# Optimization experiments

Measured on AMD Instinct MI355X. Metric: run time of the kernel, lower is better.

## Reference

```python
import jax, jax.numpy as jnp
import numpy as np
from jax import lax

# ---- static config (mirrors cfg) ----
ACT_SIZE = 768
GROUP_SIZES = [2048, 2048, 4096, 8192, 16384]
DICT_SIZE = sum(GROUP_SIZES)            # 32768
GROUP_IDX = np.concatenate([[0], np.cumsum(GROUP_SIZES)]).tolist()
TOP_K = 32
TOP_K_AUX = 512
L1_COEFF = 0.0003
AUX_PENALTY = 0.03125
N_DEAD = 5.0
THRESH_LR = 0.01
BATCH = 2048


def setup_inputs() -> dict:
    key = jax.random.key(0)
    k1, k2, k3, k4 = jax.random.split(key, 4)
    x = jax.random.normal(k1, (BATCH, ACT_SIZE), dtype=jnp.float32)
    W_enc = jax.random.normal(k2, (ACT_SIZE, DICT_SIZE), dtype=jnp.float32) * 0.02
    W_dec = jax.random.normal(k3, (DICT_SIZE, ACT_SIZE), dtype=jnp.float32)
    W_dec = W_dec / jnp.linalg.norm(W_dec, axis=-1, keepdims=True)  # unit-norm rows as in __init__
    num_batches_not_active = jax.random.randint(k4, (DICT_SIZE,), 0, 10).astype(jnp.float32)
    threshold = jnp.float32(0.0)
    return {"x": x, "W_enc": W_enc, "W_dec": W_dec, "b_dec": jnp.zeros((ACT_SIZE,), jnp.float32),
            "num_batches_not_active": num_batches_not_active, "threshold": threshold}


def reference(x, W_enc, W_dec, b_dec, num_batches_not_active, threshold):
    B, D = x.shape[0], DICT_SIZE
    # ---- preprocess (input_unit_norm=True) ----
    x_mean = x.mean(axis=-1, keepdims=True)
    x_std = jnp.std(x, axis=-1, keepdims=True, ddof=1)  # torch .std is unbiased
    xn = (x - x_mean) / (x_std + 1e-5)

    x_cent = xn - b_dec
    # ---- encode + global batch top-k (training path) ----
    acts = jax.nn.relu(x_cent @ W_enc)                  # [B, D]
    flat = acts.reshape(-1)
    k = TOP_K * B
    vals, idx = lax.top_k(flat, k)
    acts_topk = jnp.zeros_like(flat).at[idx].set(vals).reshape(B, D)

    # threshold EMA update (no_grad in torch)
    atk = lax.stop_gradient(acts_topk)
    pos = atk > 0
    min_pos = jnp.min(jnp.where(pos, atk, jnp.inf))
    new_threshold = jnp.where(pos.any(), (1 - THRESH_LR) * threshold + THRESH_LR * min_pos, threshold)

    # ---- matryoshka group decode ----
    x_reconstruct = jnp.broadcast_to(b_dec, xn.shape)
    inters = []
    for i in range(len(GROUP_SIZES)):
        s, e = GROUP_IDX[i], GROUP_IDX[i + 1]
        x_reconstruct = acts_topk[:, s:e] @ W_dec[s:e, :] + x_reconstruct
        inters.append(x_reconstruct)

    # ---- inactive-feature bookkeeping (no_grad) ----
    col_sums = lax.stop_gradient(acts_topk).sum(axis=0)
    nb = jnp.where(col_sums > 0, 0.0, num_batches_not_active + 1.0)

    # ---- loss dict ----
    total_l2 = jnp.mean((b_dec - xn) ** 2)
    l2s = jnp.stack([jnp.mean((r - xn) ** 2) for r in inters])
    total_l2 = total_l2 + l2s.sum()
    mean_l2 = total_l2 / (len(inters) + 1)
    x_var = jnp.var(xn, ddof=1)
    fvu = mean_l2 / (x_var + 1e-10)
    l1_norm = jnp.abs(acts_topk).sum(-1).mean()
    l0_norm = (acts_topk > 0).astype(jnp.float32).sum(-1).mean()
    l1_loss = L1_COEFF * l1_norm

    # ---- auxiliary loss over dead features ----
    dead = nb >= N_DEAD                                  # [D] bool, static count >> TOP_K_AUX here
    residual = xn - x_reconstruct
    masked = jnp.where(dead[None, :], acts, -jnp.inf)    # restrict top-k to dead features
    vals_a, idx_a = lax.top_k(masked, TOP_K_AUX)         # per-row top-k, [B, TOP_K_AUX]
    vals_a = jnp.where(jnp.isfinite(vals_a), vals_a, 0.0)
    acts_aux = jnp.zeros((B, D), acts.dtype).at[jnp.arange(B)[:, None], idx_a].set(vals_a)
    aux_reconstruct = acts_aux @ W_dec
    aux_mse = jnp.mean((aux_reconstruct - residual) ** 2)
    aux_loss = jnp.where(jnp.abs(aux_reconstruct).sum() > 0, AUX_PENALTY * aux_mse, 0.0)

    loss = mean_l2 + l1_loss + aux_loss
    num_dead_features = (nb > N_DEAD).sum()
    sae_out = x_reconstruct * x_std + x_mean

    return (sae_out, acts_topk, loss, l1_loss, mean_l2, l2s.min(), l2s.max(),
            l0_norm, l1_norm, aux_loss, new_threshold, fvu, num_dead_features)
```

## Files before the change

kernel.cpp:

```cpp
#include <hip/hip_runtime.h>
#include <stdint.h>

#define DEVFN static __device__ __forceinline__

typedef unsigned short u16;
typedef unsigned long long u64;
typedef short short8 __attribute__((ext_vector_type(8)));
typedef float vf4 __attribute__((ext_vector_type(4)));

constexpr int B = 2048;
constexpr int DIN = 768;
constexpr int D = 32768;
constexpr int NDI = B * D;
constexpr unsigned TOPK_TOTAL = 65536u;
constexpr int TOPK_AUX = 512;
constexpr int ROWCAP = 512;
constexpr int CANDCAP = 2097152;
constexpr int CSTAGE = 4096;
constexpr int TIECAP = 4096;
constexpr int SCAP = 3072;
constexpr int NREP = 16;

constexpr size_t OFF_HIST1  = 0;
constexpr size_t OFF_HIST2  = 131072;
constexpr size_t OFF_HIST3  = 262144;
constexpr size_t OFF_HIST4  = 393216;
constexpr size_t OFF_SCALU  = 458752;
constexpr size_t OFF_SCALD  = 459008;
constexpr size_t OFF_ROWCNT = 459264;
constexpr size_t OFF_AUXCNT = 467456;
constexpr size_t OFF_COLACT = 475648;
constexpr size_t ZERO_BYTES = 606720;
constexpr size_t OFF_XN    = ZERO_BYTES;
constexpr size_t OFF_RES   = OFF_XN   + 6291456;
constexpr size_t OFF_RMEAN = OFF_RES  + 6291456;
constexpr size_t OFF_RSTD  = OFF_RMEAN + 8192;
constexpr size_t OFF_XNCB  = OFF_RSTD + 8192;
constexpr size_t OFF_DEAD  = OFF_XNCB + 3145728;
constexpr size_t OFF_DMASK = OFF_DEAD + 131072;
constexpr size_t OFF_DBASE = OFF_DMASK + 4096;
constexpr size_t OFF_RLC   = OFF_DBASE + 2048;
constexpr size_t OFF_RLV   = OFF_RLC  + 4194304;
constexpr size_t OFF_AXC   = OFF_RLV  + 4194304;
constexpr size_t OFF_AXV   = OFF_AXC  + 4194304;
constexpr size_t OFF_CANDI = OFF_AXV  + 4194304;
constexpr size_t OFF_CANDV = OFF_CANDI + (size_t)CANDCAP * 4;
constexpr size_t OFF_TIEB  = OFF_CANDV + (size_t)CANDCAP * 4;
constexpr size_t OFF_WT    = OFF_TIEB + (size_t)TIECAP * 4;


DEVFN u16 f2bf(float f) {
  unsigned u = __float_as_uint(f);
  unsigned r = (u + 0x7FFFu + ((u >> 16) & 1u)) >> 16;
  return (u16)r;
}
DEVFN float b2f(u16 h) { return __uint_as_float(((unsigned)h) << 16); }

DEVFN float bsumf(float v, float* red) {
  int t = threadIdx.x;
  red[t] = v; __syncthreads();
  for (int o = 128; o > 0; o >>= 1) { if (t < o) red[t] += red[t + o]; __syncthreads(); }
  float r = red[0]; __syncthreads();
  return r;
}
DEVFN unsigned bsumu(unsigned v, unsigned* red) {
  int t = threadIdx.x;
  red[t] = v; __syncthreads();
  for (int o = 128; o > 0; o >>= 1) { if (t < o) red[t] += red[t + o]; __syncthreads(); }
  unsigned r = red[0]; __syncthreads();
  return r;
}

DEVFN void findBin(const unsigned* hist, int nb, unsigned K, unsigned base,
                   unsigned* sscan, int* s_b, unsigned* s_cnt)
{
  int t = threadIdx.x;
  int chunk = nb >> 8;
  int hi = nb - 1 - t * chunk;
  unsigned p = 0;
  for (int k = 0; k < chunk; ++k) p += hist[hi - k];
  sscan[t] = p; __syncthreads();
  for (int o = 1; o < 256; o <<= 1) {
    unsigned xx = (t >= o) ? sscan[t - o] : 0u; __syncthreads();
    sscan[t] += xx; __syncthreads();
  }
  unsigned incl = sscan[t], excl = incl - p;
  unsigned cum = base + excl;
  if (base + incl >= K && cum < K) {
    unsigned acc = cum;
    for (int k = 0; k < chunk; ++k) {
      unsigned h = hist[hi - k];
      if (acc + h >= K) { *s_b = hi - k; *s_cnt = acc; break; }
      acc += h;
    }
  }
  __syncthreads();
}

__global__ __launch_bounds__(256) void k_rowstats(
    const float* __restrict__ x, const float* __restrict__ bdec,
    float* __restrict__ xn, u16* __restrict__ xncb,
    float* __restrict__ rmean, float* __restrict__ rstd, double* scalD)
{
  __shared__ float red[256];
  const int row = blockIdx.x, t = threadIdx.x;
  const float* xr = x + (size_t)row * DIN;
  float v0 = xr[t], v1 = xr[t + 256], v2 = xr[t + 512];
  float mean = bsumf(v0 + v1 + v2, red) * (1.0f / DIN);
  float d0 = v0 - mean, d1 = v1 - mean, d2 = v2 - mean;
  float var = bsumf(d0 * d0 + d1 * d1 + d2 * d2, red) * (1.0f / (DIN - 1));
  float sd = sqrtf(var);
  float inv = 1.0f / (sd + 1e-5f);
  float n0 = d0 * inv, n1 = d1 * inv, n2 = d2 * inv;
  size_t o = (size_t)row * DIN;
  xn[o + t] = n0; xn[o + t + 256] = n1; xn[o + t + 512] = n2;
  float b0 = bdec[t], b1 = bdec[t + 256], b2 = bdec[t + 512];
  xncb[o + t] = f2bf(n0 - b0); xncb[o + t + 256] = f2bf(n1 - b1); xncb[o + t + 512] = f2bf(n2 - b2);
  if (t == 0) { rmean[row] = mean; rstd[row] = sd; }
  float sxn = bsumf(n0 + n1 + n2, red);
  float ssq = bsumf(n0 * n0 + n1 * n1 + n2 * n2, red);
  float e0 = b0 - n0, e1 = b1 - n1, e2 = b2 - n2;
  float sq0 = bsumf(e0 * e0 + e1 * e1 + e2 * e2, red);
  if (t == 0) {
    atomicAdd(&scalD[1], (double)sxn);
    atomicAdd(&scalD[2], (double)ssq);
    atomicAdd(&scalD[3], (double)sq0);
  }
}

__global__ __launch_bounds__(256) void k_wt(const float* __restrict__ W, u16* __restrict__ Wt)
{
  __shared__ float tl[64][65];
  const int t = threadIdx.x;
  const int n0 = blockIdx.x * 64, k0 = blockIdx.y * 64;
  const int rr = t >> 6, cc = t & 63;
#pragma unroll
  for (int r = 0; r < 16; ++r) {
    int kk = r * 4 + rr;
    tl[kk][cc] = W[(size_t)(k0 + kk) * D + n0 + cc];
  }
  __syncthreads();
#pragma unroll
  for (int r = 0; r < 16; ++r) {
    int nn = r * 4 + rr;
    Wt[(size_t)(n0 + nn) * DIN + k0 + cc] = f2bf(tl[cc][nn]);
  }
}

__global__ __launch_bounds__(256) void k_wdecb(const float4* __restrict__ W4, u16* __restrict__ Wb)
{
  int stride = gridDim.x * blockDim.x;
  const int n4 = (D * DIN) / 4;
  for (int i = blockIdx.x * 256 + threadIdx.x; i < n4; i += stride) {
    float4 f = W4[i];
    unsigned p0 = (unsigned)f2bf(f.x) | ((unsigned)f2bf(f.y) << 16);
    unsigned p1 = (unsigned)f2bf(f.z) | ((unsigned)f2bf(f.w) << 16);
    uint2 q; q.x = p0; q.y = p1;
    *(uint2*)&Wb[(size_t)i * 4] = q;
  }
}

__global__ __launch_bounds__(256) void k_gemm(const u16* __restrict__ A,
                                              const u16* __restrict__ Bt,
                                              float* __restrict__ C,
                                              unsigned* __restrict__ hist16)
{
  __shared__ __align__(16) char lds[32768];
  const int tid = threadIdx.x, lane = tid & 63, wid = tid >> 6;
  const int bn = blockIdx.x * 128, bm = blockIdx.y * 128;

  const char* pA[4]; const char* pB[4];
#pragma unroll
  for (int i = 0; i < 4; ++i) {
    int G = i * 256 + wid * 64 + lane;
    int r = G >> 3, c = (G & 7) ^ (r & 7);
    pA[i] = (const char*)(A + (size_t)(bm + r) * DIN + c * 8);
    pB[i] = (const char*)(Bt + (size_t)(bn + r) * DIN + c * 8);
  }
  int aoff[2][4], boff[2][4];
#pragma unroll
  for (int kc = 0; kc < 2; ++kc)
#pragma unroll
    for (int i = 0; i < 4; ++i) {
      int cs = kc * 4 + (lane >> 4);
      int rA = (wid >> 1) * 64 + i * 16 + (lane & 15);
      aoff[kc][i] = rA * 128 + ((cs ^ (rA & 7)) * 16);
      int rB = (wid & 1) * 64 + i * 16 + (lane & 15);
      boff[kc][i] = 16384 + rB * 128 + ((cs ^ (rB & 7)) * 16);
    }

  vf4 acc[4][4];
#pragma unroll
  for (int i = 0; i < 4; ++i)
#pragma unroll
    for (int j = 0; j < 4; ++j) acc[i][j] = (vf4)0.f;

  for (int ks = 0; ks < 12; ++ks) {
    __syncthreads();
#pragma unroll
    for (int i = 0; i < 4; ++i) {
      __builtin_amdgcn_global_load_lds(
          (const __attribute__((address_space(1))) void*)pA[i],
          (__attribute__((address_space(3))) void*)(lds + (i * 256 + wid * 64) * 16), 16, 0, 0);
      __builtin_amdgcn_global_load_lds(
          (const __attribute__((address_space(1))) void*)pB[i],
          (__attribute__((address_space(3))) void*)(lds + 16384 + (i * 256 + wid * 64) * 16), 16, 0, 0);
      pA[i] += 128; pB[i] += 128;
    }
    __syncthreads();
#pragma unroll
    for (int kc = 0; kc < 2; ++kc) {
      short8 av[4], bv[4];
#pragma unroll
      for (int i = 0; i < 4; ++i) {
        av[i] = *(const short8*)(lds + aoff[kc][i]);
        bv[i] = *(const short8*)(lds + boff[kc][i]);
      }
#pragma unroll
      for (int i = 0; i < 4; ++i)
#pragma unroll
        for (int j = 0; j < 4; ++j)
          acc[i][j] = __builtin_amdgcn_mfma_f32_16x16x32_bf16(av[i], bv[j], acc[i][j], 0, 0, 0);
    }
  }

  unsigned* h = (unsigned*)lds;
  __syncthreads();
  for (int j = tid; j < 2048; j += 256) h[j] = 0;
  __syncthreads();

  const int r0 = bm + (wid >> 1) * 64 + (lane >> 4) * 4;
  const int c0 = bn + (wid & 1) * 64 + (lane & 15);
#pragma unroll
  for (int i = 0; i < 4; ++i)
#pragma unroll
    for (int j = 0; j < 4; ++j) {
      float* cp = C + (size_t)(r0 + i * 16) * D + c0 + j * 16;
#pragma unroll
      for (int q = 0; q < 4; ++q) {
        float v = fmaxf(acc[i][j][q], 0.f);
        cp[(size_t)q * D] = v;
        if (v >= 1.0f) atomicAdd(&h[__float_as_uint(v) >> 21], 1u);
      }
    }
  __syncthreads();
  unsigned* dst = hist16 + (size_t)(blockIdx.x & (NREP - 1)) * 2048;
  for (int j = 508 + tid; j < 2048; j += 256) {
    unsigned c = h[j];
    if (c) atomicAdd(&dst[j], c);
  }
}

__global__ __launch_bounds__(256) void k_scan1a(unsigned* scalU, const unsigned* __restrict__ h16)
{
  __shared__ unsigned hsum[2048];
  __shared__ unsigned sscan[256];
  __shared__ int s_b; __shared__ unsigned s_cnt;
  int t = threadIdx.x;
  for (int j = t; j < 2048; j += 256) {
    unsigned s = 0;
#pragma unroll
    for (int r = 0; r < NREP; ++r) s += h16[r * 2048 + j];
    hsum[j] = s;
  }
  if (t == 0) { s_b = 0; s_cnt = 0; }
  __syncthreads();
  unsigned p = 0;
  for (int j = 508 + t; j < 2048; j += 256) p += hsum[j];
  unsigned total = bsumu(p, sscan);
  if (total >= TOPK_TOTAL) {
    findBin(hsum, 2048, TOPK_TOTAL, 0u, sscan, &s_b, &s_cnt);
    if (t == 0) { scalU[0] = (unsigned)s_b; scalU[1] = s_cnt; scalU[13] = 0u; }
  } else if (t == 0) scalU[13] = 1u;
}

__global__ __launch_bounds__(256) void k_histfull(const float4* __restrict__ a4,
    const unsigned* __restrict__ scalU, unsigned* __restrict__ h16)
{
  if (scalU[13] == 0u) return;
  __shared__ unsigned lh[4][2048];
  for (int j = threadIdx.x; j < 8192; j += 256) ((unsigned*)lh)[j] = 0;
  __syncthreads();
  unsigned* mylh = lh[threadIdx.x & 3];
  int stride = gridDim.x * blockDim.x;
  for (int i = blockIdx.x * 256 + threadIdx.x; i < NDI / 4; i += stride) {
    float4 f = a4[i];
    if (f.x > 0.f) atomicAdd(&mylh[__float_as_uint(f.x) >> 21], 1u);
    if (f.y > 0.f) atomicAdd(&mylh[__float_as_uint(f.y) >> 21], 1u);
    if (f.z > 0.f) atomicAdd(&mylh[__float_as_uint(f.z) >> 21], 1u);
    if (f.w > 0.f) atomicAdd(&mylh[__float_as_uint(f.w) >> 21], 1u);
  }
  __syncthreads();
  unsigned* dst = h16 + (size_t)(blockIdx.x & (NREP - 1)) * 2048;
  for (int j = threadIdx.x; j < 2048; j += 256) {
    unsigned c = lh[0][j] + lh[1][j] + lh[2][j] + lh[3][j];
    if (c) atomicAdd(&dst[j], c);
  }
}

__global__ __launch_bounds__(256) void k_scan1b(unsigned* scalU, const unsigned* __restrict__ h16)
{
  if (scalU[13] == 0u) return;
  __shared__ unsigned hsum[2048];
  __shared__ unsigned sscan[256];
  __shared__ int s_b; __shared__ unsigned s_cnt;
  int t = threadIdx.x;
  for (int j = t; j < 2048; j += 256) {
    unsigned s = 0;
#pragma unroll
    for (int r = 0; r < NREP; ++r) s += h16[r * 2048 + j];
    hsum[j] = s;
  }
  if (t == 0) { s_b = 0; s_cnt = 0; }
  __syncthreads();
  findBin(hsum, 2048, TOPK_TOTAL, 0u, sscan, &s_b, &s_cnt);
  if (t == 0) { scalU[0] = (unsigned)s_b; scalU[1] = s_cnt; }
}

__global__ __launch_bounds__(256) void k_compact(const float4* __restrict__ a4,
    unsigned* scalU, unsigned* __restrict__ candI, float* __restrict__ candV)
{
  __shared__ unsigned sIdx[CSTAGE];
  __shared__ float sVal[CSTAGE];
  __shared__ unsigned sCnt, sBase;
  if (threadIdx.x == 0) sCnt = 0;
  __syncthreads();
  unsigned b1 = scalU[0];
  int stride = gridDim.x * blockDim.x;
  for (int i = blockIdx.x * 256 + threadIdx.x; i < NDI / 4; i += stride) {
    float4 f = a4[i];
    float vv[4] = {f.x, f.y, f.z, f.w};
#pragma unroll
    for (int c = 0; c < 4; ++c) {
      float v = vv[c];
      if (v > 0.f && (__float_as_uint(v) >> 21) >= b1) {
        unsigned p = atomicAdd(&sCnt, 1u);
        if (p < (unsigned)CSTAGE) { sIdx[p] = (unsigned)(i * 4 + c); sVal[p] = v; }
        else {
          unsigned g = atomicAdd(&scalU[12], 1u);
          if (g < (unsigned)CANDCAP) { candI[g] = (unsigned)(i * 4 + c); candV[g] = v; }
        }
      }
    }
  }
  __syncthreads();
  unsigned n = sCnt < (unsigned)CSTAGE ? sCnt : (unsigned)CSTAGE;
  if (threadIdx.x == 0) sBase = atomicAdd(&scalU[12], n);
  __syncthreads();
  unsigned base = sBase;
  for (unsigned j = threadIdx.x; j < n; j += 256) {
    unsigned g = base + j;
    if (g < (unsigned)CANDCAP) { candI[g] = sIdx[j]; candV[g] = sVal[j]; }
  }
}

__global__ __launch_bounds__(256) void k_rhist2(const unsigned* __restrict__ scalU,
    const float* __restrict__ candV, unsigned* __restrict__ h16)
{
  __shared__ unsigned lh[2048];
  for (int j = threadIdx.x; j < 2048; j += 256) lh[j] = 0;
  __syncthreads();
  unsigned b1 = scalU[0];
  int n = (int)scalU[12]; if (n > CANDCAP) n = CANDCAP;
  int stride = gridDim.x * blockDim.x;
  for (int j = blockIdx.x * 256 + threadIdx.x; j < n; j += stride) {
    unsigned u = __float_as_uint(candV[j]);
    if ((u >> 21) == b1) atomicAdd(&lh[(u >> 10) & 0x7FFu], 1u);
  }
  __syncthreads();
  unsigned* dst = h16 + (size_t)(blockIdx.x & (NREP - 1)) * 2048;
  for (int j = threadIdx.x; j < 2048; j += 256) {
    unsigned c = lh[j];
    if (c) atomicAdd(&dst[j], c);
  }
}

__global__ __launch_bounds__(256) void k_rscan2(unsigned* scalU, const unsigned* __restrict__ h16)
{
  __shared__ unsigned hsum[2048];
  __shared__ unsigned sscan[256];
  __shared__ int s_b; __shared__ unsigned s_cnt;
  int t = threadIdx.x;
  for (int j = t; j < 2048; j += 256) {
    unsigned s = 0;
#pragma unroll
    for (int r = 0; r < NREP; ++r) s += h16[r * 2048 + j];
    hsum[j] = s;
  }
  if (t == 0) { s_b = 0; s_cnt = 0; }
  __syncthreads();
  findBin(hsum, 2048, TOPK_TOTAL, scalU[1], sscan, &s_b, &s_cnt);
  if (t == 0) { scalU[2] = (unsigned)s_b; scalU[3] = s_cnt; }
}

__global__ __launch_bounds__(256) void k_rhist3(const unsigned* __restrict__ scalU,
    const float* __restrict__ candV, unsigned* __restrict__ h16)
{
  __shared__ unsigned lh[1024];
  for (int j = threadIdx.x; j < 1024; j += 256) lh[j] = 0;
  __syncthreads();
  unsigned b1 = scalU[0], b2 = scalU[2];
  int n = (int)scalU[12]; if (n > CANDCAP) n = CANDCAP;
  int stride = gridDim.x * blockDim.x;
  for (int j = blockIdx.x * 256 + threadIdx.x; j < n; j += stride) {
    unsigned u = __float_as_uint(candV[j]);
    if ((u >> 21) == b1 && ((u >> 10) & 0x7FFu) == b2) atomicAdd(&lh[u & 0x3FFu], 1u);
  }
  __syncthreads();
  unsigned* dst = h16 + (size_t)(blockIdx.x & (NREP - 1)) * 1024;
  for (int j = threadIdx.x; j < 1024; j += 256) {
    unsigned c = lh[j];
    if (c) atomicAdd(&dst[j], c);
  }
}

__global__ __launch_bounds__(256) void k_rscan3(unsigned* scalU, const unsigned* __restrict__ h16)
{
  __shared__ unsigned hsum[1024];
  __shared__ unsigned sscan[256];
  __shared__ int s_b; __shared__ unsigned s_cnt;
  int t = threadIdx.x;
  for (int j = t; j < 1024; j += 256) {
    unsigned s = 0;
#pragma unroll
    for (int r = 0; r < NREP; ++r) s += h16[r * 1024 + j];
    hsum[j] = s;
  }
  if (t == 0) { s_b = 0; s_cnt = 0; }
  __syncthreads();
  findBin(hsum, 1024, TOPK_TOTAL, scalU[3], sscan, &s_b, &s_cnt);
  if (t == 0) {
    unsigned cut = (scalU[0] << 21) | (scalU[2] << 10) | (unsigned)s_b;
    scalU[4] = cut; scalU[5] = s_cnt; scalU[6] = TOPK_TOTAL - s_cnt;
  }
}

__global__ __launch_bounds__(256) void k_tiecol(unsigned* scalU,
    const unsigned* __restrict__ candI, const float* __restrict__ candV,
    unsigned* __restrict__ tieB)
{
  unsigned cut = scalU[4];
  int n = (int)scalU[12]; if (n > CANDCAP) n = CANDCAP;
  int stride = gridDim.x * blockDim.x;
  for (int j = blockIdx.x * 256 + threadIdx.x; j < n; j += stride) {
    if (__float_as_uint(candV[j]) == cut) {
      unsigned p = atomicAdd(&scalU[14], 1u);
      if (p < (unsigned)TIECAP) tieB[p] = candI[j];
    }
  }
}

__global__ __launch_bounds__(256) void k_tieres(unsigned* scalU, const unsigned* __restrict__ tieB)
{
  __shared__ unsigned tbuf[TIECAP];
  __shared__ int sthr;
  int t = threadIdx.x;
  int m = (int)scalU[14]; if (m > TIECAP) m = TIECAP;
  int need = (int)scalU[6];
  for (int j = t; j < m; j += 256) tbuf[j] = tieB[j];
  if (t == 0) sthr = 0x7FFFFFFF;
  __syncthreads();
  if (need < m) {
    for (int ci = t; ci < m; ci += 256) {
      unsigned me = tbuf[ci];
      int r = 0;
      for (int j = 0; j < m; ++j) r += (tbuf[j] < me) ? 1 : 0;
      if (r == need - 1) sthr = (int)me;
    }
  }
  __syncthreads();
  if (t == 0) scalU[7] = (unsigned)sthr;
}

__global__ __launch_bounds__(256) void k_s1b(unsigned* scalU,
    const unsigned* __restrict__ candI, const float* __restrict__ candV,
    unsigned* rowCnt, unsigned* rlc, float* rlv, unsigned* colAct, double* scalD)
{
  __shared__ float redf[256];
  __shared__ unsigned redu[256];
  unsigned cut = scalU[4]; int tthr = (int)scalU[7];
  int n = (int)scalU[12]; if (n > CANDCAP) n = CANDCAP;
  float l1 = 0.f; unsigned l0 = 0;
  int stride = gridDim.x * blockDim.x;
  for (int j = blockIdx.x * 256 + threadIdx.x; j < n; j += stride) {
    float v = candV[j];
    unsigned u = __float_as_uint(v);
    unsigned idx = candI[j];
    if (u > cut || (u == cut && (int)idx <= tthr)) {
      int row = (int)(idx >> 15), col = (int)(idx & (D - 1));
      unsigned slot = atomicAdd(&rowCnt[row], 1u);
      if (slot < ROWCAP) {
        rlc[(size_t)row * ROWCAP + slot] = (unsigned)col;
        rlv[(size_t)row * ROWCAP + slot] = v;
      }
      colAct[col] = 1u;
      l1 += v; l0++;
    }
  }
  float l1s = bsumf(l1, redf);
  unsigned l0s = bsumu(l0, redu);
  if (threadIdx.x == 0) { atomicAdd(&scalD[0], (double)l1s); atomicAdd(&scalU[9], l0s); }
}

__global__ __launch_bounds__(256) void k_scatter(const unsigned* __restrict__ scalU,
    const unsigned* __restrict__ candI, const float* __restrict__ candV, float* __restrict__ acts)
{
  unsigned cut = scalU[4]; int tthr = (int)scalU[7];
  int n = (int)scalU[12]; if (n > CANDCAP) n = CANDCAP;
  int stride = gridDim.x * blockDim.x;
  for (int j = blockIdx.x * 256 + threadIdx.x; j < n; j += stride) {
    float v = candV[j];
    unsigned u = __float_as_uint(v);
    unsigned idx = candI[j];
    if (u > cut || (u == cut && (int)idx <= tthr)) acts[idx] = v;
  }
}

__global__ __launch_bounds__(256) void k_dead(const unsigned* __restrict__ colAct,
    const float* __restrict__ nbna, unsigned* deadCols, unsigned* scalU,
    u64* __restrict__ dmask, unsigned* __restrict__ dbase)
{
  __shared__ unsigned scan[256];
  __shared__ unsigned svd;
  const int t = threadIdx.x;
  if (t == 0) svd = 0;
  __syncthreads();
  const int c0 = t * 128;
  u64 w0 = 0, w1 = 0;
  unsigned vd = 0;
  for (int i = 0; i < 64; ++i) {
    int c = c0 + i;
    bool act = colAct[c] != 0;
    float f = nbna[c] + 1.0f;
    if (!act && f >= 5.0f) w0 |= (1ull << i);
    vd += (!act && f > 5.0f) ? 1u : 0u;
  }
  for (int i = 0; i < 64; ++i) {
    int c = c0 + 64 + i;
    bool act = colAct[c] != 0;
    float f = nbna[c] + 1.0f;
    if (!act && f >= 5.0f) w1 |= (1ull << i);
    vd += (!act && f > 5.0f) ? 1u : 0u;
  }
  unsigned cnt = (unsigned)(__popcll(w0) + __popcll(w1));
  scan[t] = cnt; __syncthreads();
  for (int o = 1; o < 256; o <<= 1) {
    unsigned xx = (t >= o) ? scan[t - o] : 0u; __syncthreads();
    scan[t] += xx; __syncthreads();
  }
  unsigned p = scan[t] - cnt;
  dmask[2 * t] = w0; dmask[2 * t + 1] = w1;
  dbase[2 * t] = p; dbase[2 * t + 1] = p + (unsigned)__popcll(w0);
  atomicAdd(&svd, vd);
  __syncthreads();
  if (t == 255) scalU[10] = scan[255];
  if (t == 0) scalU[11] = svd;
  (void)deadCols;
}

__global__ __launch_bounds__(256) void k_auxsel(const float* __restrict__ acts,
    const unsigned* __restrict__ scalU, const u64* __restrict__ dmask,
    unsigned* auxC, float* auxV, unsigned* auxN)
{
  __shared__ u64 smask[512];
  __shared__ unsigned hist[2048];
  __shared__ unsigned sscan[256];
  __shared__ float tval[SCAP];
  __shared__ unsigned tcol[SCAP];
  __shared__ int s_b; __shared__ unsigned s_cnt;
  __shared__ unsigned s_sel, s_tm;
  const int row = blockIdx.x, t = threadIdx.x;
  const float4* arow4 = (const float4*)(acts + (size_t)row * D);

  for (int j = t; j < 512; j += 256) smask[j] = dmask[j];
  for (int j = t; j < 2048; j += 256) hist[j] = 0;
  if (t == 0) { s_sel = 0; s_tm = 0; s_b = 0; s_cnt = 0; }
  __syncthreads();

  unsigned pcnt = 0;
  for (int j = t; j < D / 4; j += 256) {
    float4 f = arow4[j];
    u64 w = smask[j >> 4];
    int sh = (j & 15) * 4;
    float vv[4] = {f.x, f.y, f.z, f.w};
#pragma unroll
    for (int c = 0; c < 4; ++c) {
      if (((w >> (sh + c)) & 1ull) && vv[c] > 0.f) {
        pcnt++;
        atomicAdd(&hist[__float_as_uint(vv[c]) >> 21], 1u);
      }
    }
  }
  unsigned P = bsumu(pcnt, sscan);
  unsigned* outC = auxC + (size_t)row * TOPK_AUX;
  float* outV = auxV + (size_t)row * TOPK_AUX;

  if (P <= (unsigned)TOPK_AUX) {
    for (int j = t; j < D / 4; j += 256) {
      float4 f = arow4[j];
      u64 w = smask[j >> 4];
      int sh = (j & 15) * 4;
      float vv[4] = {f.x, f.y, f.z, f.w};
#pragma unroll
      for (int c = 0; c < 4; ++c)
        if (((w >> (sh + c)) & 1ull) && vv[c] > 0.f) {
          unsigned s = atomicAdd(&s_sel, 1u);
          outC[s] = (unsigned)(j * 4 + c); outV[s] = vv[c];
        }
    }
    __syncthreads();
    if (t == 0) auxN[row] = s_sel;
    return;
  }

  __syncthreads();
  findBin(hist, 2048, (unsigned)TOPK_AUX, 0u, sscan, &s_b, &s_cnt);
  unsigned b1 = (unsigned)s_b, c1 = s_cnt;

  for (int j = t; j < D / 4; j += 256) {
    float4 f = arow4[j];
    u64 w = smask[j >> 4];
    int sh = (j & 15) * 4;
    float vv[4] = {f.x, f.y, f.z, f.w};
#pragma unroll
    for (int c = 0; c < 4; ++c) {
      if (((w >> (sh + c)) & 1ull) && vv[c] > 0.f) {
        unsigned bin = __float_as_uint(vv[c]) >> 21;
        if (bin > b1) {
          unsigned s = atomicAdd(&s_sel, 1u);
          outC[s] = (unsigned)(j * 4 + c); outV[s] = vv[c];
        } else if (bin == b1) {
          unsigned p = atomicAdd(&s_tm, 1u);
          if (p < (unsigned)SCAP) { tcol[p] = (unsigned)(j * 4 + c); tval[p] = vv[c]; }
        }
      }
    }
  }
  __syncthreads();
  int m = (int)s_tm;

  if (m <= SCAP) {
    for (int j = t; j < 2048; j += 256) hist[j] = 0;
    if (t == 0) { s_b = 0; s_cnt = 0; }
    __syncthreads();
    for (int j = t; j < m; j += 256)
      atomicAdd(&hist[(__float_as_uint(tval[j]) >> 10) & 0x7FFu], 1u);
    __syncthreads();
    findBin(hist, 2048, (unsigned)TOPK_AUX, c1, sscan, &s_b, &s_cnt);
    unsigned b2 = (unsigned)s_b, c2 = s_cnt;
    for (int j = t; j < 1024; j += 256) hist[j] = 0;
    if (t == 0) { s_b = 0; s_cnt = 0; }
    __syncthreads();
    for (int j = t; j < m; j += 256) {
      unsigned u = __float_as_uint(tval[j]);
      if (((u >> 10) & 0x7FFu) == b2) atomicAdd(&hist[u & 0x3FFu], 1u);
    }
    __syncthreads();
    findBin(hist, 1024, (unsigned)TOPK_AUX, c2, sscan, &s_b, &s_cnt);
    unsigned cut = (b1 << 21) | (b2 << 10) | (unsigned)s_b;
    int need = TOPK_AUX - (int)s_cnt;
    for (int j = t; j < m; j += 256) {
      unsigned u = __float_as_uint(tval[j]);
      if (u > cut) {
        unsigned s = atomicAdd(&s_sel, 1u);
        outC[s] = tcol[j]; outV[s] = tval[j];
      } else if (u == cut) {
        unsigned col = tcol[j];
        int r = 0;
        for (int k = 0; k < m; ++k)
          r += (__float_as_uint(tval[k]) == cut && tcol[k] < col) ? 1 : 0;
        if (r < need) { unsigned s = atomicAdd(&s_sel, 1u); outC[s] = col; outV[s] = tval[j]; }
      }
    }
    __syncthreads();
    if (t == 0) auxN[row] = s_sel;
    return;
  }

  for (int j = t; j < 2048; j += 256) hist[j] = 0;
  if (t == 0) { s_b = 0; s_cnt = 0; }
  __syncthreads();
  for (int j = t; j < D / 4; j += 256) {
    float4 f = arow4[j];
    u64 w = smask[j >> 4];
    int sh = (j & 15) * 4;
    float vv[4] = {f.x, f.y, f.z, f.w};
#pragma unroll
    for (int c = 0; c < 4; ++c) {
      if (((w >> (sh + c)) & 1ull) && vv[c] > 0.f) {
        unsigned u = __float_as_uint(vv[c]);
        if ((u >> 21) == b1) atomicAdd(&hist[(u >> 10) & 0x7FFu], 1u);
      }
    }
  }
  __syncthreads();
  findBin(hist, 2048, (unsigned)TOPK_AUX, c1, sscan, &s_b, &s_cnt);
  unsigned b2 = (unsigned)s_b, c2 = s_cnt;
  for (int j = t; j < 1024; j += 256) hist[j] = 0;
  if (t == 0) { s_b = 0; s_cnt = 0; }
  __syncthreads();
  unsigned hi21 = (b1 << 11) | b2;
  for (int j = t; j < D / 4; j += 256) {
    float4 f = arow4[j];
    u64 w = smask[j >> 4];
    int sh = (j & 15) * 4;
    float vv[4] = {f.x, f.y, f.z, f.w};
#pragma unroll
    for (int c = 0; c < 4; ++c) {
      if (((w >> (sh + c)) & 1ull) && vv[c] > 0.f) {
        unsigned u = __float_as_uint(vv[c]);
        if ((u >> 10) == hi21) atomicAdd(&hist[u & 0x3FFu], 1u);
      }
    }
  }
  __syncthreads();
  findBin(hist, 1024, (unsigned)TOPK_AUX, c2, sscan, &s_b, &s_cnt);
  unsigned cut = (b1 << 21) | (b2 << 10) | (unsigned)s_b;
  int need = TOPK_AUX - (int)s_cnt;
  if (t == 0) s_tm = 0;
  __syncthreads();
  for (int j = t; j < D / 4; j += 256) {
    float4 f = arow4[j];
    u64 w = smask[j >> 4];
    int sh = (j & 15) * 4;
    float vv[4] = {f.x, f.y, f.z, f.w};
#pragma unroll
    for (int c = 0; c < 4; ++c) {
      if (((w >> (sh + c)) & 1ull) && vv[c] > 0.f) {
        unsigned u = __float_as_uint(vv[c]);
        if (u > cut && (u >> 21) == b1) {
          unsigned s = atomicAdd(&s_sel, 1u);
          outC[s] = (unsigned)(j * 4 + c); outV[s] = vv[c];
        } else if (u == cut) {
          unsigned p = atomicAdd(&s_tm, 1u);
          if (p < (unsigned)SCAP) tcol[p] = (unsigned)(j * 4 + c);
        }
      }
    }
  }
  __syncthreads();
  int mm = (int)s_tm; if (mm > SCAP) mm = SCAP;
  float cv = __uint_as_float(cut);
  for (int ci = t; ci < mm; ci += 256) {
    unsigned col = tcol[ci];
    int r = 0;
    for (int j = 0; j < mm; ++j) r += (tcol[j] < col) ? 1 : 0;
    if (r < need) { unsigned s = atomicAdd(&s_sel, 1u); outC[s] = col; outV[s] = cv; }
  }
  __syncthreads();
  if (t == 0) auxN[row] = s_sel;
}

__global__ __launch_bounds__(256) void k_decode(const u16* __restrict__ Wdecb,
    const float* __restrict__ bdec, const float* __restrict__ xn,
    const unsigned* __restrict__ rowCnt, const unsigned* __restrict__ rlc,
    const float* __restrict__ rlv, const float* __restrict__ rmean,
    const float* __restrict__ rstd, float* __restrict__ sae,
    float* __restrict__ resid, double* scalD)
{
  __shared__ int tlc[ROWCAP]; __shared__ float tlv[ROWCAP];
  __shared__ int slc[ROWCAP]; __shared__ float slv[ROWCAP];
  __shared__ int gcnt[5], gpos[5], gend[5];
  __shared__ float red[256];
  const int row = blockIdx.x, t = threadIdx.x;
  int cnt = (int)rowCnt[row]; if (cnt > ROWCAP) cnt = ROWCAP;
  if (t < 5) gcnt[t] = 0;
  __syncthreads();
  for (int e = t; e < cnt; e += 256) {
    int c = (int)rlc[(size_t)row * ROWCAP + e];
    tlc[e] = c; tlv[e] = rlv[(size_t)row * ROWCAP + e];
    int ilog = 31 - __clz(c | 1);
    int g = ilog > 10 ? ilog - 10 : 0;
    atomicAdd(&gcnt[g], 1);
  }
  __syncthreads();
  if (t == 0) {
    int b = 0;
    for (int g = 0; g < 5; ++g) { gpos[g] = b; b += gcnt[g]; gend[g] = b; }
  }
  __syncthreads();
  for (int e = t; e < cnt; e += 256) {
    int c = tlc[e];
    int ilog = 31 - __clz(c | 1);
    int g = ilog > 10 ? ilog - 10 : 0;
    int p = atomicAdd(&gpos[g], 1);
    slc[p] = c; slv[p] = tlv[e];
  }
  __syncthreads();
  float r0 = bdec[t], r1 = bdec[t + 256], r2 = bdec[t + 512];
  size_t o = (size_t)row * DIN;
  float x0 = xn[o + t], x1 = xn[o + t + 256], x2 = xn[o + t + 512];
  int e = 0;
#pragma unroll 1
  for (int g = 0; g < 5; ++g) {
    int e1 = gend[g];
#pragma unroll 2
    for (; e < e1; ++e) {
      int c = slc[e]; float v = slv[e];
      const u16* w = Wdecb + (size_t)c * DIN;
      r0 = fmaf(v, b2f(w[t]), r0);
      r1 = fmaf(v, b2f(w[t + 256]), r1);
      r2 = fmaf(v, b2f(w[t + 512]), r2);
    }
    float dd0 = r0 - x0, dd1 = r1 - x1, dd2 = r2 - x2;
    float sq = bsumf(dd0 * dd0 + dd1 * dd1 + dd2 * dd2, red);
    if (t == 0) atomicAdd(&scalD[4 + g], (double)sq);
  }
  float m = rmean[row], sd = rstd[row];
  sae[o + t] = r0 * sd + m; sae[o + t + 256] = r1 * sd + m; sae[o + t + 512] = r2 * sd + m;
  resid[o + t] = x0 - r0; resid[o + t + 256] = x1 - r1; resid[o + t + 512] = x2 - r2;
}

__global__ __launch_bounds__(256) void k_auxdec(const u16* __restrict__ Wdecb,
    const unsigned* __restrict__ auxC, const float* __restrict__ auxV,
    const unsigned* __restrict__ auxN, const float* __restrict__ resid, double* scalD)
{
  __shared__ int lc[TOPK_AUX]; __shared__ float lv[TOPK_AUX];
  __shared__ float red[256];
  const int row = blockIdx.x, t = threadIdx.x;
  int cnt = (int)auxN[row]; if (cnt > TOPK_AUX) cnt = TOPK_AUX;
  for (int e = t; e < cnt; e += 256) {
    lc[e] = (int)auxC[(size_t)row * TOPK_AUX + e];
    lv[e] = auxV[(size_t)row * TOPK_AUX + e];
  }
  __syncthreads();
  float a0 = 0.f, a1 = 0.f, a2 = 0.f;
#pragma unroll 4
  for (int e = 0; e < cnt; ++e) {
    int c = lc[e]; float v = lv[e];
    const u16* w = Wdecb + (size_t)c * DIN;
    a0 = fmaf(v, b2f(w[t]), a0);
    a1 = fmaf(v, b2f(w[t + 256]), a1);
    a2 = fmaf(v, b2f(w[t + 512]), a2);
  }
  size_t o = (size_t)row * DIN;
  float s0 = resid[o + t], s1 = resid[o + t + 256], s2 = resid[o + t + 512];
  float d0 = a0 - s0, d1 = a1 - s1, d2 = a2 - s2;
  float sq = bsumf(d0 * d0 + d1 * d1 + d2 * d2, red);
  float ab = bsumf(fabsf(a0) + fabsf(a1) + fabsf(a2), red);
  if (t == 0) { atomicAdd(&scalD[9], (double)sq); atomicAdd(&scalD[10], (double)ab); }
}

__global__ void k_final(const unsigned* __restrict__ scalU, const double* __restrict__ scalD,
                        const float* __restrict__ thr, float* __restrict__ out)
{
  if (threadIdx.x != 0 || blockIdx.x != 0) return;
  const double NEL = (double)B * (double)DIN;
  double term0 = scalD[3] / NEL;
  double tot = term0;
  double mn = 1e300, mx = -1e300;
  for (int g = 0; g < 5; ++g) {
    double l2 = scalD[4 + g] / NEL;
    tot += l2;
    mn = l2 < mn ? l2 : mn;
    mx = l2 > mx ? l2 : mx;
  }
  double mean_l2 = tot / 6.0;
  double sum = scalD[1], ssq = scalD[2];
  double xvar = (ssq - sum * sum / NEL) / (NEL - 1.0);
  double fvu = mean_l2 / (xvar + 1e-10);
  double l1n = scalD[0] / (double)B;
  double l1loss = (double)0.0003f * l1n;
  double l0n = (double)scalU[9] / (double)B;
  double auxmse = scalD[9] / NEL;
  double auxloss = (scalD[10] > 0.0) ? 0.03125 * auxmse : 0.0;
  double loss = mean_l2 + l1loss + auxloss;
  float cutv = __uint_as_float(scalU[4]);
  float t0 = thr[0];
  float newthr = (scalU[9] > 0u) ? (0.99f * t0 + 0.01f * cutv) : t0;
  float* s = out + (size_t)B * DIN + (size_t)NDI;
  s[0] = (float)loss;   s[1] = (float)l1loss; s[2] = (float)mean_l2;
  s[3] = (float)mn;     s[4] = (float)mx;     s[5] = (float)l0n;
  s[6] = (float)l1n;    s[7] = (float)auxloss; s[8] = newthr;
  s[9] = (float)fvu;    s[10] = (float)scalU[11];
}

extern "C" void kernel_launch(void* const* d_in, const int* in_sizes, int n_in,
                              void* d_out, int out_size, void* d_ws, size_t ws_size,
                              hipStream_t stream)
{
  (void)in_sizes; (void)n_in; (void)out_size; (void)ws_size;
  const float* x    = (const float*)d_in[0];
  const float* Wenc = (const float*)d_in[1];
  const float* Wdec = (const float*)d_in[2];
  const float* bdec = (const float*)d_in[3];
  const float* nbna = (const float*)d_in[4];
  const float* thr  = (const float*)d_in[5];
  float* out = (float*)d_out;
  char* ws = (char*)d_ws;

  float* sae  = out;
  float* acts = out + (size_t)B * DIN;

  unsigned* hist1 = (unsigned*)(ws + OFF_HIST1);
  unsigned* hist2 = (unsigned*)(ws + OFF_HIST2);
  unsigned* hist3 = (unsigned*)(ws + OFF_HIST3);
  unsigned* hist4 = (unsigned*)(ws + OFF_HIST4);
  unsigned* scalU = (unsigned*)(ws + OFF_SCALU);
  double*   scalD = (double*)(ws + OFF_SCALD);
  unsigned* rowCnt= (unsigned*)(ws + OFF_ROWCNT);
  unsigned* auxN  = (unsigned*)(ws + OFF_AUXCNT);
  unsigned* colAct= (unsigned*)(ws + OFF_COLACT);
  float* xn    = (float*)(ws + OFF_XN);
  float* resid = (float*)(ws + OFF_RES);
  float* rmean = (float*)(ws + OFF_RMEAN);
  float* rstd  = (float*)(ws + OFF_RSTD);
  u16*   xncb  = (u16*)(ws + OFF_XNCB);
  unsigned* deadC = (unsigned*)(ws + OFF_DEAD);
  u64*      dmask = (u64*)(ws + OFF_DMASK);
  unsigned* dbase = (unsigned*)(ws + OFF_DBASE);
  unsigned* rlc = (unsigned*)(ws + OFF_RLC);
  float*    rlv = (float*)(ws + OFF_RLV);
  unsigned* auxC = (unsigned*)(ws + OFF_AXC);
  float*    auxV = (float*)(ws + OFF_AXV);
  unsigned* candI = (unsigned*)(ws + OFF_CANDI);
  float*    candV = (float*)(ws + OFF_CANDV);
  unsigned* tieB  = (unsigned*)(ws + OFF_TIEB);
  u16* Wt    = (u16*)(ws + OFF_WT);
  u16* Wdecb = (u16*)(ws + OFF_WT);

  hipMemsetAsync(ws, 0, ZERO_BYTES, stream);
  hipLaunchKernelGGL(k_rowstats, dim3(B), dim3(256), 0, stream, x, bdec, xn, xncb, rmean, rstd, scalD);
  hipLaunchKernelGGL(k_wt, dim3(D / 64, DIN / 64), dim3(256), 0, stream, Wenc, Wt);
  hipLaunchKernelGGL(k_gemm, dim3(D / 128, B / 128), dim3(256), 0, stream, xncb, Wt, acts, hist1);
  hipLaunchKernelGGL(k_scan1a, dim3(1), dim3(256), 0, stream, scalU, hist1);
  hipLaunchKernelGGL(k_histfull, dim3(2048), dim3(256), 0, stream, (const float4*)acts, scalU, hist2);
  hipLaunchKernelGGL(k_scan1b, dim3(1), dim3(256), 0, stream, scalU, hist2);
  hipLaunchKernelGGL(k_wdecb, dim3(2048), dim3(256), 0, stream, (const float4*)Wdec, Wdecb);
  hipLaunchKernelGGL(k_compact, dim3(2048), dim3(256), 0, stream, (const float4*)acts, scalU, candI, candV);
  hipLaunchKernelGGL(k_rhist2, dim3(256), dim3(256), 0, stream, scalU, candV, hist3);
  hipLaunchKernelGGL(k_rscan2, dim3(1), dim3(256), 0, stream, scalU, hist3);
  hipLaunchKernelGGL(k_rhist3, dim3(256), dim3(256), 0, stream, scalU, candV, hist4);
  hipLaunchKernelGGL(k_rscan3, dim3(1), dim3(256), 0, stream, scalU, hist4);
  hipLaunchKernelGGL(k_tiecol, dim3(256), dim3(256), 0, stream, scalU, candI, candV, tieB);
  hipLaunchKernelGGL(k_tieres, dim3(1), dim3(256), 0, stream, scalU, tieB);
  hipLaunchKernelGGL(k_s1b, dim3(256), dim3(256), 0, stream, scalU, candI, candV, rowCnt, rlc, rlv, colAct, scalD);
  hipLaunchKernelGGL(k_dead, dim3(1), dim3(256), 0, stream, colAct, nbna, deadC, scalU, dmask, dbase);
  hipLaunchKernelGGL(k_auxsel, dim3(B), dim3(256), 0, stream, acts, scalU, dmask, auxC, auxV, auxN);
  hipMemsetAsync(acts, 0, (size_t)NDI * 4, stream);
  hipLaunchKernelGGL(k_scatter, dim3(256), dim3(256), 0, stream, scalU, candI, candV, acts);
  hipLaunchKernelGGL(k_decode, dim3(B), dim3(256), 0, stream, Wdecb, bdec, xn, rowCnt, rlc, rlv, rmean, rstd, sae, resid, scalD);
  hipLaunchKernelGGL(k_auxdec, dim3(B), dim3(256), 0, stream, Wdecb, auxC, auxV, auxN, resid, scalD);
  hipLaunchKernelGGL(k_final, dim3(1), dim3(64), 0, stream, scalU, scalD, thr, out);
}
```

Measured before the change: 920.4 us.

## Fuse top-k candidate compaction into GEMM epilogue and swap grid order

The GEMM epilogue now writes every activation at or above 1.0 into the global candidate list through an LDS staging buffer with one global atomic per block. The full-matrix compaction pass then runs only as a fallback when too few candidates exceed 1.0, which removes a 256MB read of acts in the common case. The grid axes are also swapped so consecutive blocks walk along M, which changes cache reuse of the weight tiles. The cost is a larger candidate list, since every value of at least 1.0 is kept instead of only those in the selected bin, which can make the later radix passes over candV heavier.

```diff
diff --git a/kernel.cpp b/kernel.cpp
--- a/kernel.cpp
+++ b/kernel.cpp
@@ -15,7 +15,8 @@
 constexpr unsigned TOPK_TOTAL = 65536u;
 constexpr int TOPK_AUX = 512;
 constexpr int ROWCAP = 512;
-constexpr int CANDCAP = 2097152;
+constexpr int CANDCAP = 3145728;
+constexpr int GSTAGE = 2048;
 constexpr int CSTAGE = 4096;
 constexpr int TIECAP = 4096;
 constexpr int SCAP = 3072;
@@ -163,11 +164,15 @@
 __global__ __launch_bounds__(256) void k_gemm(const u16* __restrict__ A,
                                               const u16* __restrict__ Bt,
                                               float* __restrict__ C,
-                                              unsigned* __restrict__ hist16)
+                                              unsigned* __restrict__ hist16,
+                                              unsigned* __restrict__ scalU,
+                                              unsigned* __restrict__ candI,
+                                              float* __restrict__ candV)
 {
   __shared__ __align__(16) char lds[32768];
+  __shared__ unsigned sCnt, sBase;
   const int tid = threadIdx.x, lane = tid & 63, wid = tid >> 6;
-  const int bn = blockIdx.x * 128, bm = blockIdx.y * 128;
+  const int bm = blockIdx.x * 128, bn = blockIdx.y * 128;
 
   const char* pA[4]; const char* pB[4];
 #pragma unroll
@@ -225,8 +230,11 @@
   }
 
   unsigned* h = (unsigned*)lds;
+  unsigned* stIdx = (unsigned*)(lds + 8192);
+  float* stVal = (float*)(lds + 16384);
   __syncthreads();
   for (int j = tid; j < 2048; j += 256) h[j] = 0;
+  if (tid == 0) sCnt = 0;
   __syncthreads();
 
   const int r0 = bm + (wid >> 1) * 64 + (lane >> 4) * 4;
@@ -240,7 +248,16 @@
       for (int q = 0; q < 4; ++q) {
         float v = fmaxf(acc[i][j][q], 0.f);
         cp[(size_t)q * D] = v;
-        if (v >= 1.0f) atomicAdd(&h[__float_as_uint(v) >> 21], 1u);
+        if (v >= 1.0f) {
+          atomicAdd(&h[__float_as_uint(v) >> 21], 1u);
+          unsigned idx = ((unsigned)(r0 + i * 16 + q) << 15) | (unsigned)(c0 + j * 16);
+          unsigned p = atomicAdd(&sCnt, 1u);
+          if (p < (unsigned)GSTAGE) { stIdx[p] = idx; stVal[p] = v; }
+          else {
+            unsigned g = atomicAdd(&scalU[12], 1u);
+            if (g < (unsigned)CANDCAP) { candI[g] = idx; candV[g] = v; }
+          }
+        }
       }
     }
   __syncthreads();
@@ -248,6 +265,14 @@
   for (int j = 508 + tid; j < 2048; j += 256) {
     unsigned c = h[j];
     if (c) atomicAdd(&dst[j], c);
+  }
+  unsigned n = sCnt < (unsigned)GSTAGE ? sCnt : (unsigned)GSTAGE;
+  if (tid == 0) sBase = atomicAdd(&scalU[12], n);
+  __syncthreads();
+  unsigned base = sBase;
+  for (unsigned jj = tid; jj < n; jj += 256) {
+    unsigned g = base + jj;
+    if (g < (unsigned)CANDCAP) { candI[g] = stIdx[jj]; candV[g] = stVal[jj]; }
   }
 }
 
@@ -271,7 +296,7 @@
   if (total >= TOPK_TOTAL) {
     findBin(hsum, 2048, TOPK_TOTAL, 0u, sscan, &s_b, &s_cnt);
     if (t == 0) { scalU[0] = (unsigned)s_b; scalU[1] = s_cnt; scalU[13] = 0u; }
-  } else if (t == 0) scalU[13] = 1u;
+  } else if (t == 0) { scalU[13] = 1u; scalU[12] = 0u; }
 }
 
 __global__ __launch_bounds__(256) void k_histfull(const float4* __restrict__ a4,
@@ -320,6 +345,7 @@
 __global__ __launch_bounds__(256) void k_compact(const float4* __restrict__ a4,
     unsigned* scalU, unsigned* __restrict__ candI, float* __restrict__ candV)
 {
+  if (scalU[13] == 0u) return;
   __shared__ unsigned sIdx[CSTAGE];
   __shared__ float sVal[CSTAGE];
   __shared__ unsigned sCnt, sBase;
@@ -922,12 +948,12 @@
   hipMemsetAsync(ws, 0, ZERO_BYTES, stream);
   hipLaunchKernelGGL(k_rowstats, dim3(B), dim3(256), 0, stream, x, bdec, xn, xncb, rmean, rstd, scalD);
   hipLaunchKernelGGL(k_wt, dim3(D / 64, DIN / 64), dim3(256), 0, stream, Wenc, Wt);
-  hipLaunchKernelGGL(k_gemm, dim3(D / 128, B / 128), dim3(256), 0, stream, xncb, Wt, acts, hist1);
+  hipLaunchKernelGGL(k_gemm, dim3(B / 128, D / 128), dim3(256), 0, stream, xncb, Wt, acts, hist1, scalU, candI, candV);
   hipLaunchKernelGGL(k_scan1a, dim3(1), dim3(256), 0, stream, scalU, hist1);
   hipLaunchKernelGGL(k_histfull, dim3(2048), dim3(256), 0, stream, (const float4*)acts, scalU, hist2);
   hipLaunchKernelGGL(k_scan1b, dim3(1), dim3(256), 0, stream, scalU, hist2);
+  hipLaunchKernelGGL(k_compact, dim3(2048), dim3(256), 0, stream, (const float4*)acts, scalU, candI, candV);
   hipLaunchKernelGGL(k_wdecb, dim3(2048), dim3(256), 0, stream, (const float4*)Wdec, Wdecb);
-  hipLaunchKernelGGL(k_compact, dim3(2048), dim3(256), 0, stream, (const float4*)acts, scalU, candI, candV);
   hipLaunchKernelGGL(k_rhist2, dim3(256), dim3(256), 0, stream, scalU, candV, hist3);
   hipLaunchKernelGGL(k_rscan2, dim3(1), dim3(256), 0, stream, scalU, hist3);
   hipLaunchKernelGGL(k_rhist3, dim3(256), dim3(256), 0, stream, scalU, candV, hist4);
```

Result: slower. 977.7 us (+6.2%).
